# Kernel optimization log

Measured on AMD Instinct MI355X. Metric: run time of the kernel, lower is better.

## Reference

```python
import jax, jax.numpy as jnp
import numpy as np
import math

D_MODEL = 512
N_HEADS = 8
D_FF = 2048
E_LAYERS = 2
ENC_IN = 3
MA_K = 25            # moving_avg kernel size
FACTOR = 1
B, L_CYC, CDL = 16, 20, 128
SEQ = L_CYC * CDL    # 2560
TOP_K = int(FACTOR * math.log(SEQ))  # 7
OUTPUT_NUM = 1


def moving_avg(x, k=MA_K):
    # x: [B,S,D]; replicate-pad ends by (k-1)//2, stride-1 mean pool -> length S
    p = (k - 1) // 2
    xp = jnp.concatenate([jnp.repeat(x[:, :1], p, axis=1), x, jnp.repeat(x[:, -1:], p, axis=1)], axis=1)
    c = jnp.cumsum(xp, axis=1)
    c = jnp.concatenate([jnp.zeros_like(c[:, :1]), c], axis=1)
    return (c[:, k:] - c[:, :-k]) / k


def token_embed(x, W):
    # x: [B,S,C], W: [D_MODEL, C, 3]; Conv1d k=3, circular padding, no bias
    xc = jnp.pad(x.transpose(0, 2, 1), ((0, 0), (0, 0), (1, 1)), mode='wrap')
    y = jax.lax.conv_general_dilated(xc, W, (1,), 'VALID', dimension_numbers=('NCH', 'OIH', 'NCH'))
    return y.transpose(0, 2, 1)  # [B,S,D]


def autocorrelation(q, k, v):
    # q,k,v: [B,S,H,E]; FFT autocorrelation + top-k time-delay aggregation (inference path)
    B_, S, H, E = q.shape
    qf = jnp.fft.rfft(q.transpose(0, 2, 3, 1), axis=-1)      # [B,H,E,F]
    kf = jnp.fft.rfft(k.transpose(0, 2, 3, 1), axis=-1)
    corr = jnp.fft.irfft(qf * jnp.conj(kf), n=S, axis=-1)    # [B,H,E,S]
    vals = v.transpose(0, 2, 3, 1)                           # [B,H,E,S]
    mean_corr = corr.mean(axis=(1, 2))                       # [B,S]
    weights, delay = jax.lax.top_k(mean_corr, TOP_K)         # [B,K]
    w = jax.nn.softmax(weights, axis=-1)

    def agg_one(v_b, d_b, w_b):
        # roll by -delay == gather values at index (t + delay) mod S
        out = jnp.zeros_like(v_b)
        for i in range(TOP_K):
            out = out + jnp.roll(v_b, -d_b[i], axis=-1) * w_b[i]
        return out

    V = jax.vmap(agg_one)(vals, delay, w)                    # [B,H,E,S]
    return V.transpose(0, 3, 1, 2)                           # [B,S,H,E]


def my_layernorm(x, g, b):
    # LayerNorm over last dim, then subtract the per-series (time) mean
    mu = x.mean(-1, keepdims=True)
    var = ((x - mu) ** 2).mean(-1, keepdims=True)
    xh = (x - mu) / jnp.sqrt(var + 1e-5) * g + b
    return xh - xh.mean(axis=1, keepdims=True)


def encoder_layer(x, Wq, bq, Wk, bk, Wv, bv, Wo, bo, Wc1, Wc2):
    B_, S, D = x.shape
    H, E = N_HEADS, D // N_HEADS
    q = (x @ Wq + bq).reshape(B_, S, H, E)
    k = (x @ Wk + bk).reshape(B_, S, H, E)
    v = (x @ Wv + bv).reshape(B_, S, H, E)
    att = autocorrelation(q, k, v).reshape(B_, S, D)
    x = x + (att @ Wo + bo)
    x = x - moving_avg(x)                                    # series_decomp1: residual part
    y = jax.nn.gelu(x @ Wc1, approximate=False) @ Wc2        # 1x1 convs, no bias
    z = x + y
    return z - moving_avg(z)                                 # series_decomp2


def setup_inputs() -> dict:
    key = jax.random.key(0)
    ks = jax.random.split(key, 12)
    s = 0.02
    rn = lambda k, shape: jax.random.normal(k, shape, dtype=jnp.float32) * s
    return {
        'cycle_curve_data': jax.random.normal(ks[0], (B, L_CYC, ENC_IN, CDL), dtype=jnp.float32),
        'curve_attn_mask': jnp.ones((B, L_CYC), dtype=jnp.float32),
        'W_emb': rn(ks[1], (D_MODEL, ENC_IN, 3)),
        'Wq': rn(ks[2], (E_LAYERS, D_MODEL, D_MODEL)),
        'bq': jnp.zeros((E_LAYERS, D_MODEL), jnp.float32),
        'Wk': rn(ks[3], (E_LAYERS, D_MODEL, D_MODEL)),
        'bk': jnp.zeros((E_LAYERS, D_MODEL), jnp.float32),
        'Wv': rn(ks[4], (E_LAYERS, D_MODEL, D_MODEL)),
        'bv': jnp.zeros((E_LAYERS, D_MODEL), jnp.float32),
        'Wo': rn(ks[5], (E_LAYERS, D_MODEL, D_MODEL)),
        'bo': jnp.zeros((E_LAYERS, D_MODEL), jnp.float32),
        'Wc1': rn(ks[6], (E_LAYERS, D_MODEL, D_FF)),
        'Wc2': rn(ks[7], (E_LAYERS, D_FF, D_MODEL)),
        'gamma': jnp.ones((D_MODEL,), jnp.float32),
        'beta': jnp.zeros((D_MODEL,), jnp.float32),
        'Wp': rn(ks[8], (D_MODEL * SEQ, OUTPUT_NUM)),
        'bp': jnp.zeros((OUTPUT_NUM,), jnp.float32),
    }


def reference(cycle_curve_data, curve_attn_mask, W_emb, Wq, bq, Wk, bk, Wv, bv, Wo, bo, Wc1, Wc2, gamma, beta, Wp, bp):
    mask = curve_attn_mask[:, :, None, None]                 # [B,L,1,1]
    x = jnp.where(mask == 0, 0.0, cycle_curve_data)          # zero masked cycles
    Bn = x.shape[0]
    x = x.transpose(0, 1, 3, 2).reshape(Bn, SEQ, ENC_IN)     # [B, L*CDL, NV]
    h = token_embed(x, W_emb)                                # DataEmbedding_wo_pos (x_mark=None, dropout=0)
    for l in range(E_LAYERS):
        h = encoder_layer(h, Wq[l], bq[l], Wk[l], bk[l], Wv[l], bv[l], Wo[l], bo[l], Wc1[l], Wc2[l])
    h = my_layernorm(h, gamma, beta)
    out = jax.nn.gelu(h, approximate=False)
    emb = out.reshape(Bn, -1)
    return emb @ Wp + bp                                     # [B, OUTPUT_NUM]
```

## Files before the change

### kernel.cpp

```cpp
#include <hip/hip_runtime.h>
#include <math.h>

#define BATCH 16
#define L_CYC 20
#define CDL 128
#define SEQ 2560
#define ENC_IN 3
#define DMODEL 512
#define DFF 2048
#define NLAYERS 2
#define TOPK 7
#define MROWS (BATCH*SEQ)
#define SD ((size_t)BATCH * SEQ * DMODEL)
#define FFN_CHUNK 20480
#define CHUNK_D 256
#define DGRP 8
#define FFT_NT 512

typedef short bf16x8 __attribute__((ext_vector_type(8)));
typedef float f32x4 __attribute__((ext_vector_type(4)));

__device__ __forceinline__ float gelu_f(float x) {
    return 0.5f * x * (1.0f + erff(x * 0.70710678118654752f));
}
__device__ __forceinline__ unsigned short f2bf(float f) {
    unsigned int u = __float_as_uint(f);
    u += 0x7fff + ((u >> 16) & 1);
    return (unsigned short)(u >> 16);
}
__device__ __forceinline__ float bf2f(unsigned short h) {
    return __uint_as_float(((unsigned int)h) << 16);
}
__device__ __forceinline__ void xcd_map(int p, int G, int& g, int& n) {
    int a = p >> 3;
    n = a % G;
    g = (a / G) * 8 + (p & 7);
}

__global__ __launch_bounds__(256) void embed_kernel(
    const float* __restrict__ data, const float* __restrict__ mask,
    const float* __restrict__ Wemb, float* __restrict__ h) {
    __shared__ float xv[9];
    size_t idx = (size_t)blockIdx.x * 256 + threadIdx.x;
    size_t r = idx >> 9;
    int s = (int)(r % SEQ);
    int b = (int)(r / SEQ);
    int tid = threadIdx.x;
    if (tid < 9) {
        int t = tid / 3, c = tid % 3;
        int u = s - 1 + t;
        if (u < 0) u += SEQ;
        if (u >= SEQ) u -= SEQ;
        int cyc = u >> 7, pos = u & 127;
        float mk = mask[b * L_CYC + cyc];
        xv[c * 3 + t] = (mk == 0.f) ? 0.f
            : data[(((size_t)b * L_CYC + cyc) * ENC_IN + c) * CDL + pos];
    }
    __syncthreads();
    int dm = idx & (DMODEL - 1);
    float acc = 0.f;
#pragma unroll
    for (int j = 0; j < 9; j++) acc += xv[j] * Wemb[dm * 9 + j];
    h[idx] = acc;
}

__global__ void conv_split_kernel(const float* __restrict__ in,
                                  unsigned short* __restrict__ hi,
                                  unsigned short* __restrict__ lo, size_t n) {
    size_t i = ((size_t)blockIdx.x * 256 + threadIdx.x) * 4;
    if (i >= n) return;
    float4 v = *(const float4*)(in + i);
    float vv[4] = { v.x, v.y, v.z, v.w };
#pragma unroll
    for (int j = 0; j < 4; j++) {
        unsigned short h = f2bf(vv[j]);
        hi[i + j] = h;
        lo[i + j] = f2bf(vv[j] - bf2f(h));
    }
}

__global__ __launch_bounds__(256) void transpose_bf16_kernel(
    const float* __restrict__ W, unsigned short* __restrict__ Wt, int K, int N) {
    __shared__ float t[32][33];
    int n0 = blockIdx.x * 32, k0 = blockIdx.y * 32;
    int c = threadIdx.x & 31, r = threadIdx.x >> 5;
    for (int i = 0; i < 4; i++)
        t[r + i * 8][c] = W[(size_t)(k0 + r + i * 8) * N + n0 + c];
    __syncthreads();
    for (int i = 0; i < 4; i++)
        Wt[(size_t)(n0 + r + i * 8) * K + k0 + c] = f2bf(t[c][r + i * 8]);
}

__global__ __launch_bounds__(256) void transpose_split_stk_kernel(
    const float* __restrict__ W, unsigned short* __restrict__ WtH,
    unsigned short* __restrict__ WtL, int which) {
    __shared__ float t[32][33];
    int n0 = blockIdx.x * 32, k0 = blockIdx.y * 32;
    int c = threadIdx.x & 31, r = threadIdx.x >> 5;
    for (int i = 0; i < 4; i++)
        t[r + i * 8][c] = W[(size_t)(k0 + r + i * 8) * DMODEL + n0 + c];
    __syncthreads();
    for (int i = 0; i < 4; i++) {
        int n = n0 + r + i * 8;
        int row = (n & 255) + ((n >> 8) * 512) + which * 256;
        float v = t[c][r + i * 8];
        unsigned short h = f2bf(v);
        size_t o = (size_t)row * DMODEL + k0 + c;
        WtH[o] = h;
        WtL[o] = f2bf(v - bf2f(h));
    }
}

__global__ void stack_bias_kernel(const float* __restrict__ bq,
                                  const float* __restrict__ bk, float* __restrict__ bstk) {
    int i = blockIdx.x * 256 + threadIdx.x;
    if (i >= 1024) return;
    int c = i >> 9, j = i & 511;
    bstk[i] = (j < 256) ? bq[c * 256 + j] : bk[c * 256 + (j - 256)];
}

__global__ __launch_bounds__(256) void wvo_kernel(
    const float* __restrict__ Wv, const float* __restrict__ Wo,
    float* __restrict__ Wvo) {
    __shared__ float row[DMODEL];
    int k = blockIdx.x;
    int tid = threadIdx.x;
    for (int j = tid; j < DMODEL; j += 256) row[j] = Wv[(size_t)k * DMODEL + j];
    __syncthreads();
    float a0 = 0.f, a1 = 0.f;
    for (int j = 0; j < DMODEL; j++) {
        float wv = row[j];
        a0 += wv * Wo[(size_t)j * DMODEL + tid];
        a1 += wv * Wo[(size_t)j * DMODEL + tid + 256];
    }
    Wvo[(size_t)k * DMODEL + tid] = a0;
    Wvo[(size_t)k * DMODEL + tid + 256] = a1;
}

__global__ void cbias_kernel(const float* __restrict__ bv, const float* __restrict__ Wo,
                             const float* __restrict__ bo, float* __restrict__ cb) {
    int n = blockIdx.x * 256 + threadIdx.x;
    if (n >= DMODEL) return;
    float acc = bo[n];
    for (int j = 0; j < DMODEL; j++) acc += bv[j] * Wo[(size_t)j * DMODEL + n];
    cb[n] = acc;
}

#define BK 32
__global__ __launch_bounds__(256) void gemm_mfma_kernel(
    const unsigned short* __restrict__ A, const unsigned short* __restrict__ Wt,
    const float* __restrict__ bias, const float* res,
    void* Cout, int M, int N, int K, int act, int outMode, int gridN)
{
    __shared__ unsigned short As[128 * 40];
    __shared__ unsigned short Bs[128 * 40];
    int tid = threadIdx.x;
    int wave = tid >> 6, lane = tid & 63;
    int wm = wave & 1, wn = wave >> 1;
    int gblk, nblk;
    xcd_map(blockIdx.x, gridN, gblk, nblk);
    int bm = gblk * 128, bn = nblk * 128;

    int r0 = tid >> 2;
    int koff = (tid & 3) * 8;
    const unsigned short* Ag = A  + (size_t)(bm + r0) * K + koff;
    const unsigned short* Bg = Wt + (size_t)(bn + r0) * K + koff;

    f32x4 acc[4][4] = {};
    int frow = lane & 15, fk = (lane >> 4) * 8;

    for (int k0 = 0; k0 < K; k0 += BK) {
        bf16x8 a0 = *(const bf16x8*)(Ag + k0);
        bf16x8 a1 = *(const bf16x8*)(Ag + (size_t)64 * K + k0);
        bf16x8 b0 = *(const bf16x8*)(Bg + k0);
        bf16x8 b1 = *(const bf16x8*)(Bg + (size_t)64 * K + k0);
        __syncthreads();
        *(bf16x8*)&As[r0 * 40 + koff]        = a0;
        *(bf16x8*)&As[(r0 + 64) * 40 + koff] = a1;
        *(bf16x8*)&Bs[r0 * 40 + koff]        = b0;
        *(bf16x8*)&Bs[(r0 + 64) * 40 + koff] = b1;
        __syncthreads();
        bf16x8 af[4], bfv[4];
#pragma unroll
        for (int mi = 0; mi < 4; mi++)
            af[mi] = *(const bf16x8*)&As[(wm * 64 + mi * 16 + frow) * 40 + fk];
#pragma unroll
        for (int nj = 0; nj < 4; nj++)
            bfv[nj] = *(const bf16x8*)&Bs[(wn * 64 + nj * 16 + frow) * 40 + fk];
#pragma unroll
        for (int mi = 0; mi < 4; mi++)
#pragma unroll
            for (int nj = 0; nj < 4; nj++)
                acc[mi][nj] = __builtin_amdgcn_mfma_f32_16x16x32_bf16(
                    af[mi], bfv[nj], acc[mi][nj], 0, 0, 0);
    }

    int lrow = (lane >> 4) * 4, lcol = lane & 15;
#pragma unroll
    for (int mi = 0; mi < 4; mi++) {
        int row0 = bm + wm * 64 + mi * 16 + lrow;
#pragma unroll
        for (int nj = 0; nj < 4; nj++) {
            int col = bn + wn * 64 + nj * 16 + lcol;
            float bv = bias ? bias[col] : 0.f;
            f32x4 v = acc[mi][nj];
#pragma unroll
            for (int r = 0; r < 4; r++) {
                int row = row0 + r;
                float x = v[r] + bv;
                if (res) x += res[(size_t)row * N + col];
                if (act == 1) x = gelu_f(x);
                if (outMode == 0) ((float*)Cout)[(size_t)row * N + col] = x;
                else              ((unsigned short*)Cout)[(size_t)row * N + col] = f2bf(x);
            }
        }
    }
}

__global__ __launch_bounds__(256) void gemm_qk_split_kernel(
    const unsigned short* __restrict__ Ahi, const unsigned short* __restrict__ Alo,
    const unsigned short* __restrict__ Whi, const unsigned short* __restrict__ Wlo,
    const float* __restrict__ bias, float* __restrict__ Ct, int M, int K, int gridN)
{
    __shared__ unsigned short AsH[128 * 40];
    __shared__ unsigned short AsL[128 * 40];
    __shared__ unsigned short BsH[128 * 40];
    __shared__ unsigned short BsL[128 * 40];
    int tid = threadIdx.x;
    int wave = tid >> 6, lane = tid & 63;
    int wm = wave & 1, wn = wave >> 1;
    int gblk, nblk;
    xcd_map(blockIdx.x, gridN, gblk, nblk);
    int bm = gblk * 128, bn = nblk * 128;

    int r0 = tid >> 2;
    int koff = (tid & 3) * 8;
    const unsigned short* AgH = Ahi + (size_t)(bm + r0) * K + koff;
    const unsigned short* AgL = Alo + (size_t)(bm + r0) * K + koff;
    const unsigned short* BgH = Whi + (size_t)(bn + r0) * K + koff;
    const unsigned short* BgL = Wlo + (size_t)(bn + r0) * K + koff;

    f32x4 acc[4][4] = {};
    int frow = lane & 15, fk = (lane >> 4) * 8;

    for (int k0 = 0; k0 < K; k0 += BK) {
        bf16x8 ah0 = *(const bf16x8*)(AgH + k0);
        bf16x8 ah1 = *(const bf16x8*)(AgH + (size_t)64 * K + k0);
        bf16x8 al0 = *(const bf16x8*)(AgL + k0);
        bf16x8 al1 = *(const bf16x8*)(AgL + (size_t)64 * K + k0);
        bf16x8 bh0 = *(const bf16x8*)(BgH + k0);
        bf16x8 bh1 = *(const bf16x8*)(BgH + (size_t)64 * K + k0);
        bf16x8 bl0 = *(const bf16x8*)(BgL + k0);
        bf16x8 bl1 = *(const bf16x8*)(BgL + (size_t)64 * K + k0);
        __syncthreads();
        *(bf16x8*)&AsH[r0 * 40 + koff]        = ah0;
        *(bf16x8*)&AsH[(r0 + 64) * 40 + koff] = ah1;
        *(bf16x8*)&AsL[r0 * 40 + koff]        = al0;
        *(bf16x8*)&AsL[(r0 + 64) * 40 + koff] = al1;
        *(bf16x8*)&BsH[r0 * 40 + koff]        = bh0;
        *(bf16x8*)&BsH[(r0 + 64) * 40 + koff] = bh1;
        *(bf16x8*)&BsL[r0 * 40 + koff]        = bl0;
        *(bf16x8*)&BsL[(r0 + 64) * 40 + koff] = bl1;
        __syncthreads();
        bf16x8 afh[4], afl[4], bfh[4], bfl[4];
#pragma unroll
        for (int mi = 0; mi < 4; mi++) {
            int o = (wm * 64 + mi * 16 + frow) * 40 + fk;
            afh[mi] = *(const bf16x8*)&AsH[o];
            afl[mi] = *(const bf16x8*)&AsL[o];
        }
#pragma unroll
        for (int nj = 0; nj < 4; nj++) {
            int o = (wn * 64 + nj * 16 + frow) * 40 + fk;
            bfh[nj] = *(const bf16x8*)&BsH[o];
            bfl[nj] = *(const bf16x8*)&BsL[o];
        }
#pragma unroll
        for (int mi = 0; mi < 4; mi++)
#pragma unroll
            for (int nj = 0; nj < 4; nj++) {
                acc[mi][nj] = __builtin_amdgcn_mfma_f32_16x16x32_bf16(
                    afh[mi], bfh[nj], acc[mi][nj], 0, 0, 0);
                acc[mi][nj] = __builtin_amdgcn_mfma_f32_16x16x32_bf16(
                    afh[mi], bfl[nj], acc[mi][nj], 0, 0, 0);
                acc[mi][nj] = __builtin_amdgcn_mfma_f32_16x16x32_bf16(
                    afl[mi], bfh[nj], acc[mi][nj], 0, 0, 0);
            }
    }

    int lrow = (lane >> 4) * 4, lcol = lane & 15;
#pragma unroll
    for (int mi = 0; mi < 4; mi++) {
        int row0 = bm + wm * 64 + mi * 16 + lrow;
#pragma unroll
        for (int nj = 0; nj < 4; nj++) {
            int col = bn + wn * 64 + nj * 16 + lcol;
            float bv = bias ? bias[col] : 0.f;
            f32x4 v = acc[mi][nj];
#pragma unroll
            for (int r = 0; r < 4; r++)
                Ct[(size_t)col * M + row0 + r] = v[r] + bv;
        }
    }
}

template<int NT>
__device__ void fft2560(float2* bufA, float2* bufB, const float2* w512, int tid) {
    const float w5r[5] = { 1.f,  0.30901699437494742f, -0.80901699437494742f,
                          -0.80901699437494742f,  0.30901699437494742f };
    const float w5i[5] = { 0.f, -0.95105651629515357f, -0.58778525229247312f,
                           0.58778525229247312f,  0.95105651629515357f };
    __syncthreads();
    const float TWO_PI = 6.283185307179586f;
    for (int j = tid; j < SEQ; j += NT) {
        int k1 = j >> 9, n2 = j & 511;
        float ar = 0.f, ai = 0.f;
        for (int n1 = 0; n1 < 5; n1++) {
            int m = (n1 * k1) % 5;
            float2 x = bufA[n1 * 512 + n2];
            ar += x.x * w5r[m] - x.y * w5i[m];
            ai += x.x * w5i[m] + x.y * w5r[m];
        }
        float ang = -TWO_PI * (float)(n2 * k1) / 2560.0f;
        float sn, cs;
        sincosf(ang, &sn, &cs);
        bufB[j] = make_float2(ar * cs - ai * sn, ar * sn + ai * cs);
    }
    __syncthreads();
    float2* X = bufB;
    float2* Y = bufA;
    int n = 512, logs = 0;
    for (int st = 0; st < 9; st++) {
        int m = n >> 1;
        int s = 1 << logs;
        for (int t = tid; t < 1280; t += NT) {
            int sub = t >> 8;
            int r = t & 255;
            int p = r >> logs;
            int q = r & (s - 1);
            int base = sub << 9;
            float2 a = X[base + q + s * p];
            float2 b = X[base + q + s * (p + m)];
            float2 sum = make_float2(a.x + b.x, a.y + b.y);
            float2 dif = make_float2(a.x - b.x, a.y - b.y);
            float2 w = w512[p << logs];
            Y[base + q + s * (2 * p)]     = sum;
            Y[base + q + s * (2 * p + 1)] = make_float2(dif.x * w.x - dif.y * w.y,
                                                        dif.x * w.y + dif.y * w.x);
        }
        __syncthreads();
        float2* tmp = X; X = Y; Y = tmp;
        n >>= 1; logs++;
    }
}

__global__ __launch_bounds__(FFT_NT) void fft_fwd_kernel(
    const float* __restrict__ qt, const float* __restrict__ kt, float* __restrict__ Z)
{
    __shared__ float2 bufA[SEQ];
    __shared__ float2 bufB[SEQ];
    __shared__ float2 w512[256];
    int d0 = blockIdx.x * DGRP;
    int b = blockIdx.y;
    int tid = threadIdx.x;
    if (tid < 256) {
        float sn, cs;
        sincosf(-6.283185307179586f * (float)tid / 512.0f, &sn, &cs);
        w512[tid] = make_float2(cs, sn);
    }
    float accR[5], accI[5];
#pragma unroll
    for (int j = 0; j < 5; j++) { accR[j] = 0.f; accI[j] = 0.f; }

    for (int col = 0; col < DGRP; col++) {
        const float* qcol = qt + (size_t)(d0 + col) * MROWS + (size_t)b * SEQ;
        const float* kcol = kt + (size_t)(d0 + col) * MROWS + (size_t)b * SEQ;
        __syncthreads();
        for (int i = tid; i < SEQ; i += FFT_NT)
            bufA[i] = make_float2(qcol[i], kcol[i]);
        fft2560<FFT_NT>(bufA, bufB, w512, tid);
#pragma unroll
        for (int j = 0; j < 5; j++) {
            int f = tid + FFT_NT * j;
            int fpos = (f % 5) * 512 + (f / 5);
            int g = f ? (SEQ - f) : 0;
            int gpos = (g % 5) * 512 + (g / 5);
            float2 Z1 = bufA[fpos], Z2 = bufA[gpos];
            accR[j] += 0.5f * (Z1.x * Z2.y + Z1.y * Z2.x);
            accI[j] += 0.25f * ((Z1.x * Z1.x + Z1.y * Z1.y)
                              - (Z2.x * Z2.x + Z2.y * Z2.y));
        }
    }
#pragma unroll
    for (int j = 0; j < 5; j++) {
        int f = tid + FFT_NT * j;
        int fpos = (f % 5) * 512 + (f / 5);
        atomicAdd(&Z[((size_t)b * SEQ + fpos) * 2 + 0], accR[j]);
        atomicAdd(&Z[((size_t)b * SEQ + fpos) * 2 + 1], accI[j]);
    }
}

__global__ __launch_bounds__(FFT_NT) void fft_inv_kernel(
    const float* __restrict__ Z, float* __restrict__ mc)
{
    __shared__ float2 bufA[SEQ];
    __shared__ float2 bufB[SEQ];
    __shared__ float2 w512[256];
    int b = blockIdx.x;
    int tid = threadIdx.x;
    if (tid < 256) {
        float sn, cs;
        sincosf(-6.283185307179586f * (float)tid / 512.0f, &sn, &cs);
        w512[tid] = make_float2(cs, sn);
    }
    for (int i = tid; i < SEQ; i += FFT_NT) {
        int k1 = i % 5, k2 = i / 5;
        float zr = Z[((size_t)b * SEQ + k1 * 512 + k2) * 2 + 0];
        float zi = Z[((size_t)b * SEQ + k1 * 512 + k2) * 2 + 1];
        bufA[i] = make_float2(zr, -zi);
    }
    fft2560<FFT_NT>(bufA, bufB, w512, tid);
    const float scale = 1.0f / (2560.0f * 512.0f);
    for (int j = tid; j < SEQ; j += FFT_NT) {
        int k1 = j >> 9, k2 = j & 511;
        mc[(size_t)b * SEQ + k1 + 5 * k2] = bufA[j].x * scale;
    }
}

__global__ __launch_bounds__(256) void topk_kernel(
    const float* __restrict__ mc, float* __restrict__ wts, int* __restrict__ dels)
{
    __shared__ float cv[SEQ];
    __shared__ float rv[256];
    __shared__ int   ri[256];
    __shared__ float topv[TOPK];
    __shared__ int   topi[TOPK];
    int b = blockIdx.x, tid = threadIdx.x;
    for (int i = tid; i < SEQ; i += 256) cv[i] = mc[(size_t)b * SEQ + i];
    __syncthreads();
    for (int it = 0; it < TOPK; it++) {
        float bv = -2e30f; int bi = 1 << 30;
        for (int i = tid; i < SEQ; i += 256) {
            float v = cv[i];
            if (v > bv || (v == bv && i < bi)) { bv = v; bi = i; }
        }
        rv[tid] = bv; ri[tid] = bi;
        __syncthreads();
        for (int off = 128; off > 0; off >>= 1) {
            if (tid < off) {
                float v2 = rv[tid + off]; int i2 = ri[tid + off];
                if (v2 > rv[tid] || (v2 == rv[tid] && i2 < ri[tid])) {
                    rv[tid] = v2; ri[tid] = i2;
                }
            }
            __syncthreads();
        }
        if (tid == 0) { topv[it] = rv[0]; topi[it] = ri[0]; cv[ri[0]] = -1e30f; }
        __syncthreads();
    }
    if (tid == 0) {
        float mx = topv[0];
        float e[TOPK], ssum = 0.f;
        for (int i = 0; i < TOPK; i++) { e[i] = expf(topv[i] - mx); ssum += e[i]; }
        for (int i = 0; i < TOPK; i++) {
            wts[b * TOPK + i] = e[i] / ssum;
            dels[b * TOPK + i] = topi[i];
        }
    }
}

__global__ void agg_res_kernel(const float* __restrict__ u, const float* __restrict__ x,
                               const float* __restrict__ cb,
                               const float* __restrict__ wts, const int* __restrict__ dels,
                               float* __restrict__ x1) {
    size_t idx = (size_t)blockIdx.x * 256 + threadIdx.x;
    if (idx >= SD) return;
    int d = idx & (DMODEL - 1);
    size_t r = idx >> 9;
    int s = (int)(r % SEQ);
    int b = (int)(r / SEQ);
    float acc = cb[d] + x[idx];
    for (int i = 0; i < TOPK; i++) {
        int del = dels[b * TOPK + i];
        float w = wts[b * TOPK + i];
        int ss = s + del; if (ss >= SEQ) ss -= SEQ;
        acc += w * u[((size_t)b * SEQ + ss) * DMODEL + d];
    }
    x1[idx] = acc;
}

#define MA_MODE_PLAIN 0
#define MA_MODE_BF    1
#define MA_MODE_SPLIT 2
template<int MODE>
__device__ __forceinline__ void ma_run_body(
    const float* __restrict__ x, float* __restrict__ out,
    unsigned short* __restrict__ o1, unsigned short* __restrict__ o2)
{
    int tid = threadIdx.x;
    int s0 = blockIdx.x * 128;
    int d  = blockIdx.y * 256 + tid;
    int b  = blockIdx.z;
    const float* xb = x + (size_t)b * SEQ * DMODEL + d;
    float sum = 0.f;
#pragma unroll
    for (int j = -12; j <= 12; j++) {
        int ss = s0 + j;
        ss = ss < 0 ? 0 : (ss > SEQ - 1 ? SEQ - 1 : ss);
        sum += xb[(size_t)ss * DMODEL];
    }
    for (int s = s0; s < s0 + 128; s++) {
        float v = xb[(size_t)s * DMODEL] - sum * (1.0f / 25.0f);
        size_t o = ((size_t)b * SEQ + s) * DMODEL + d;
        out[o] = v;
        if (MODE == MA_MODE_BF) {
            o1[o] = f2bf(v);
        } else if (MODE == MA_MODE_SPLIT) {
            unsigned short h = f2bf(v);
            o1[o] = h;
            o2[o] = f2bf(v - bf2f(h));
        }
        int add = s + 13; if (add > SEQ - 1) add = SEQ - 1;
        int sub = s - 12; if (sub < 0) sub = 0;
        sum += xb[(size_t)add * DMODEL] - xb[(size_t)sub * DMODEL];
    }
}
__global__ __launch_bounds__(256) void ma_sub_kernel(
    const float* __restrict__ x, float* __restrict__ out) {
    ma_run_body<MA_MODE_PLAIN>(x, out, nullptr, nullptr);
}
__global__ __launch_bounds__(256) void ma_sub_bf_kernel(
    const float* __restrict__ x, float* __restrict__ out,
    unsigned short* __restrict__ obf) {
    ma_run_body<MA_MODE_BF>(x, out, obf, nullptr);
}
__global__ __launch_bounds__(256) void ma_sub_split_kernel(
    const float* __restrict__ x, float* __restrict__ out,
    unsigned short* __restrict__ hi, unsigned short* __restrict__ lo) {
    ma_run_body<MA_MODE_SPLIT>(x, out, hi, lo);
}

__global__ __launch_bounds__(256) void ln_kernel(
    const float* __restrict__ x, const float* __restrict__ g,
    const float* __restrict__ be, float* __restrict__ xh)
{
    int row = blockIdx.x;
    int tid = threadIdx.x;
    __shared__ float red[256];
    const float* xr = x + (size_t)row * DMODEL;
    float v0 = xr[tid], v1 = xr[tid + 256];
    red[tid] = v0 + v1;
    __syncthreads();
    for (int off = 128; off > 0; off >>= 1) {
        if (tid < off) red[tid] += red[tid + off];
        __syncthreads();
    }
    float mu = red[0] / (float)DMODEL;
    __syncthreads();
    float d0 = v0 - mu, d1 = v1 - mu;
    red[tid] = d0 * d0 + d1 * d1;
    __syncthreads();
    for (int off = 128; off > 0; off >>= 1) {
        if (tid < off) red[tid] += red[tid + off];
        __syncthreads();
    }
    float inv = rsqrtf(red[0] / (float)DMODEL + 1e-5f);
    xh[(size_t)row * DMODEL + tid]       = d0 * inv * g[tid] + be[tid];
    xh[(size_t)row * DMODEL + tid + 256] = d1 * inv * g[tid + 256] + be[tid + 256];
}

__global__ __launch_bounds__(256) void colmean_kernel(
    const float* __restrict__ xh, float* __restrict__ cm) {
    int idx = blockIdx.x * 256 + threadIdx.x;
    int d = idx & (DMODEL - 1), b = idx >> 9;
    int s0 = blockIdx.y * 128;
    float acc = 0.f;
    for (int s = s0; s < s0 + 128; s++)
        acc += xh[((size_t)b * SEQ + s) * DMODEL + d];
    atomicAdd(&cm[idx], acc * (1.0f / (float)SEQ));
}

__global__ __launch_bounds__(256) void final_kernel(
    const float* __restrict__ xh, const float* __restrict__ cm,
    const float* __restrict__ Wp, const float* __restrict__ bp,
    float* __restrict__ out)
{
    int b = blockIdx.y, chunk = blockIdx.x;
    int tid = threadIdx.x;
    const size_t per = (size_t)SEQ * DMODEL / 64;
    size_t start = (size_t)chunk * per;
    float acc = 0.f;
    for (size_t i = start + tid; i < start + per; i += 256) {
        int d = (int)(i & (DMODEL - 1));
        float v = xh[(size_t)b * SEQ * DMODEL + i] - cm[b * DMODEL + d];
        acc += gelu_f(v) * Wp[i];
    }
    __shared__ float red[256];
    red[tid] = acc;
    __syncthreads();
    for (int off = 128; off > 0; off >>= 1) {
        if (tid < off) red[tid] += red[tid + off];
        __syncthreads();
    }
    if (tid == 0) {
        atomicAdd(&out[b], red[0]);
        if (chunk == 0) atomicAdd(&out[b], bp[0]);
    }
}

extern "C" void kernel_launch(void* const* d_in, const int* in_sizes, int n_in,
                              void* d_out, int out_size, void* d_ws, size_t ws_size,
                              hipStream_t stream) {
    const float* data  = (const float*)d_in[0];
    const float* mask  = (const float*)d_in[1];
    const float* Wemb  = (const float*)d_in[2];
    const float* Wq    = (const float*)d_in[3];
    const float* bq    = (const float*)d_in[4];
    const float* Wk    = (const float*)d_in[5];
    const float* bk    = (const float*)d_in[6];
    const float* Wv    = (const float*)d_in[7];
    const float* bv    = (const float*)d_in[8];
    const float* Wo    = (const float*)d_in[9];
    const float* bo    = (const float*)d_in[10];
    const float* Wc1   = (const float*)d_in[11];
    const float* Wc2   = (const float*)d_in[12];
    const float* gamma = (const float*)d_in[13];
    const float* beta  = (const float*)d_in[14];
    const float* Wp    = (const float*)d_in[15];
    const float* bp    = (const float*)d_in[16];
    float* out = (float*)d_out;

    float* buf0 = (float*)d_ws;
    float* buf1 = buf0 + SD;
    float* buf2 = buf1 + SD;

    unsigned short* WstkH = (unsigned short*)(buf2 + SD);
    unsigned short* WstkL = WstkH + 2 * DMODEL * DMODEL;
    unsigned short* Wvot  = WstkL + 2 * DMODEL * DMODEL;
    unsigned short* Wc1t  = Wvot + DMODEL * DMODEL;
    unsigned short* Wc2t  = Wc1t + (size_t)DMODEL * DFF;
    float* WvoF = (float*)(Wc2t + (size_t)DMODEL * DFF);
    float* CB   = WvoF + (size_t)DMODEL * DMODEL;
    float* Bstk = CB + DMODEL;
    float* Zb = Bstk + 1024;
    float* MC = Zb + (size_t)BATCH * SEQ * 2;
    float* WT = MC + (size_t)BATCH * SEQ;
    int*   DL = (int*)(WT + BATCH * TOPK);
    float* CM = (float*)(DL + BATCH * TOPK);

    const int NB  = (int)((SD + 255) / 256);
    const int NB4 = (int)((SD / 4 + 255) / 256);
    dim3 gMA(SEQ / 128, 2, BATCH);

    float* X  = buf0;
    float* HL = buf1;
    float* S  = buf2;

    embed_kernel<<<NB, 256, 0, stream>>>(data, mask, Wemb, X);
    conv_split_kernel<<<NB4, 256, 0, stream>>>(
        X, (unsigned short*)HL + SD, (unsigned short*)HL, SD);

    const int gSqBlocks = (MROWS / 128) * (DMODEL / 128);
    const int gF1Blocks = (FFN_CHUNK / 128) * (DFF / 128);
    const int gF2Blocks = (FFN_CHUNK / 128) * (DMODEL / 128);

    for (int l = 0; l < NLAYERS; l++) {
        const float* wq = Wq + (size_t)l * DMODEL * DMODEL;
        const float* wk = Wk + (size_t)l * DMODEL * DMODEL;
        const float* wv = Wv + (size_t)l * DMODEL * DMODEL;
        const float* wo = Wo + (size_t)l * DMODEL * DMODEL;
        const float* bqL = bq + (size_t)l * DMODEL;
        const float* bkL = bk + (size_t)l * DMODEL;
        const float* bvL = bv + (size_t)l * DMODEL;
        const float* boL = bo + (size_t)l * DMODEL;
        const float* wc1 = Wc1 + (size_t)l * DMODEL * DFF;
        const float* wc2 = Wc2 + (size_t)l * DFF * DMODEL;

        unsigned short* Lbf = (unsigned short*)HL;
        unsigned short* Hbf = Lbf + SD;
        float* qtf = S;
        float* ktf = S + (size_t)MROWS * CHUNK_D;

        dim3 gT(DMODEL / 32, DMODEL / 32);
        transpose_split_stk_kernel<<<gT, 256, 0, stream>>>(wq, WstkH, WstkL, 0);
        transpose_split_stk_kernel<<<gT, 256, 0, stream>>>(wk, WstkH, WstkL, 1);
        stack_bias_kernel<<<4, 256, 0, stream>>>(bqL, bkL, Bstk);
        wvo_kernel<<<DMODEL, 256, 0, stream>>>(wv, wo, WvoF);
        transpose_bf16_kernel<<<gT, 256, 0, stream>>>(WvoF, Wvot, DMODEL, DMODEL);
        cbias_kernel<<<2, 256, 0, stream>>>(bvL, wo, boL, CB);
        transpose_bf16_kernel<<<dim3(DFF / 32, DMODEL / 32), 256, 0, stream>>>(wc1, Wc1t, DMODEL, DFF);
        transpose_bf16_kernel<<<dim3(DMODEL / 32, DFF / 32), 256, 0, stream>>>(wc2, Wc2t, DFF, DMODEL);

        hipMemsetAsync(Zb, 0, (size_t)BATCH * SEQ * 2 * sizeof(float), stream);
        for (int c = 0; c < DMODEL / CHUNK_D; c++) {
            gemm_qk_split_kernel<<<gSqBlocks, 256, 0, stream>>>(
                Hbf, Lbf, WstkH + (size_t)c * 512 * DMODEL,
                WstkL + (size_t)c * 512 * DMODEL, Bstk + c * 512,
                S, MROWS, DMODEL, DMODEL / 128);
            fft_fwd_kernel<<<dim3(CHUNK_D / DGRP, BATCH), FFT_NT, 0, stream>>>(qtf, ktf, Zb);
        }
        fft_inv_kernel<<<BATCH, FFT_NT, 0, stream>>>(Zb, MC);
        topk_kernel<<<BATCH, 256, 0, stream>>>(MC, WT, DL);

        gemm_mfma_kernel<<<gSqBlocks, 256, 0, stream>>>(Hbf, Wvot, nullptr, nullptr, S,
                                                        MROWS, DMODEL, DMODEL, 0, 0,
                                                        DMODEL / 128);
        agg_res_kernel<<<NB, 256, 0, stream>>>(S, X, CB, WT, DL, HL);
        ma_sub_bf_kernel<<<gMA, 256, 0, stream>>>(HL, X, (unsigned short*)S);
        for (int c = 0; c < MROWS / FFN_CHUNK; c++) {
            const unsigned short* x2c = (unsigned short*)S + (size_t)c * FFN_CHUNK * DMODEL;
            float* xz = X + (size_t)c * FFN_CHUNK * DMODEL;
            gemm_mfma_kernel<<<gF1Blocks, 256, 0, stream>>>(x2c, Wc1t, nullptr, nullptr,
                                                            (unsigned short*)HL,
                                                            FFN_CHUNK, DFF, DMODEL, 1, 1,
                                                            DFF / 128);
            gemm_mfma_kernel<<<gF2Blocks, 256, 0, stream>>>((unsigned short*)HL, Wc2t,
                                                            nullptr, xz, xz,
                                                            FFN_CHUNK, DMODEL, DFF, 0, 0,
                                                            DMODEL / 128);
        }
        if (l + 1 < NLAYERS)
            ma_sub_split_kernel<<<gMA, 256, 0, stream>>>(
                X, S, (unsigned short*)HL + SD, (unsigned short*)HL);
        else
            ma_sub_kernel<<<gMA, 256, 0, stream>>>(X, S);
        float* tmp = X; X = S; S = tmp;
    }

    ln_kernel<<<MROWS, 256, 0, stream>>>(X, gamma, beta, HL);
    hipMemsetAsync(CM, 0, (size_t)BATCH * DMODEL * sizeof(float), stream);
    colmean_kernel<<<dim3(32, 20), 256, 0, stream>>>(HL, CM);
    hipMemsetAsync(out, 0, (size_t)out_size * sizeof(float), stream);
    final_kernel<<<dim3(64, BATCH), 256, 0, stream>>>(HL, CM, Wp, bp, out);
}
```

Measured before the change: 2.272 ms.

## Rewrite FFT-2560 core with radix-4 stages, swizzled LDS and precomputed twiddles

Replaces the nine radix-2 stages of the 512-point sub-FFTs with four radix-4 stages plus one final radix-2 stage. This halves the number of barrier-separated LDS passes. LDS indices go through an XOR swizzle to cut bank conflicts. The per-element sincosf in the radix-5 pass is replaced by per-thread twiddles computed once, and the radix-5 pass is unrolled so each thread handles its five inputs in registers. The cost is more index arithmetic and a new output ordering that must line up with the later consumers.

```diff
diff --git a/kernel.cpp b/kernel.cpp
--- a/kernel.cpp
+++ b/kernel.cpp
@@ -304,54 +304,90 @@
     }
 }
 
+__device__ __forceinline__ int swz(int a) { return a ^ ((a >> 4) & 15); }
+
+template<int LOGS, int NT>
+__device__ __forceinline__ void radix4_stage(const float2* __restrict__ X,
+                                             float2* __restrict__ Y,
+                                             const float2* __restrict__ w512x,
+                                             int tid) {
+    const int s = 1 << LOGS;
+    for (int t = tid; t < 640; t += NT) {
+        int sub = t >> 7, r = t & 127;
+        int base = sub << 9;
+        int q = r & (s - 1);
+        int ps = r - q;
+        float2 x0 = X[swz(base + r)];
+        float2 x1 = X[swz(base + r + 128)];
+        float2 x2 = X[swz(base + r + 256)];
+        float2 x3 = X[swz(base + r + 384)];
+        float A0r = x0.x + x2.x, A0i = x0.y + x2.y;
+        float B0r = x1.x + x3.x, B0i = x1.y + x3.y;
+        float A1r = x0.x - x2.x, A1i = x0.y - x2.y;
+        float B1r = x1.x - x3.x, B1i = x1.y - x3.y;
+        float2 w1 = w512x[ps];
+        float w2r = w1.x * w1.x - w1.y * w1.y;
+        float w2i = 2.0f * w1.x * w1.y;
+        float w3r = w2r * w1.x - w2i * w1.y;
+        float w3i = w2r * w1.y + w2i * w1.x;
+        float u1r = A1r + B1i, u1i = A1i - B1r;
+        float u2r = A0r - B0r, u2i = A0i - B0i;
+        float u3r = A1r - B1i, u3i = A1i + B1r;
+        int ob = base + q + 4 * ps;
+        Y[swz(ob)]         = make_float2(A0r + B0r, A0i + B0i);
+        Y[swz(ob + s)]     = make_float2(u1r * w1.x - u1i * w1.y,
+                                         u1r * w1.y + u1i * w1.x);
+        Y[swz(ob + 2 * s)] = make_float2(u2r * w2r - u2i * w2i,
+                                         u2r * w2i + u2i * w2r);
+        Y[swz(ob + 3 * s)] = make_float2(u3r * w3r - u3i * w3i,
+                                         u3r * w3i + u3i * w3r);
+    }
+}
+
 template<int NT>
-__device__ void fft2560(float2* bufA, float2* bufB, const float2* w512, int tid) {
-    const float w5r[5] = { 1.f,  0.30901699437494742f, -0.80901699437494742f,
-                          -0.80901699437494742f,  0.30901699437494742f };
-    const float w5i[5] = { 0.f, -0.95105651629515357f, -0.58778525229247312f,
-                           0.58778525229247312f,  0.95105651629515357f };
-    __syncthreads();
-    const float TWO_PI = 6.283185307179586f;
-    for (int j = tid; j < SEQ; j += NT) {
-        int k1 = j >> 9, n2 = j & 511;
-        float ar = 0.f, ai = 0.f;
-        for (int n1 = 0; n1 < 5; n1++) {
-            int m = (n1 * k1) % 5;
-            float2 x = bufA[n1 * 512 + n2];
-            ar += x.x * w5r[m] - x.y * w5i[m];
-            ai += x.x * w5i[m] + x.y * w5r[m];
-        }
-        float ang = -TWO_PI * (float)(n2 * k1) / 2560.0f;
-        float sn, cs;
-        sincosf(ang, &sn, &cs);
-        bufB[j] = make_float2(ar * cs - ai * sn, ar * sn + ai * cs);
-    }
-    __syncthreads();
-    float2* X = bufB;
-    float2* Y = bufA;
-    int n = 512, logs = 0;
-    for (int st = 0; st < 9; st++) {
-        int m = n >> 1;
-        int s = 1 << logs;
-        for (int t = tid; t < 1280; t += NT) {
-            int sub = t >> 8;
-            int r = t & 255;
-            int p = r >> logs;
-            int q = r & (s - 1);
-            int base = sub << 9;
-            float2 a = X[base + q + s * p];
-            float2 b = X[base + q + s * (p + m)];
-            float2 sum = make_float2(a.x + b.x, a.y + b.y);
-            float2 dif = make_float2(a.x - b.x, a.y - b.y);
-            float2 w = w512[p << logs];
-            Y[base + q + s * (2 * p)]     = sum;
-            Y[base + q + s * (2 * p + 1)] = make_float2(dif.x * w.x - dif.y * w.y,
-                                                        dif.x * w.y + dif.y * w.x);
-        }
-        __syncthreads();
-        float2* tmp = X; X = Y; Y = tmp;
-        n >>= 1; logs++;
-    }
+__device__ void fft2560(float2* bufA, float2* bufB, const float2* w512x,
+                        const float2* tw, int tid) {
+    __syncthreads();
+    {
+        const float w5r[5] = { 1.f,  0.30901699437494742f, -0.80901699437494742f,
+                              -0.80901699437494742f,  0.30901699437494742f };
+        const float w5i[5] = { 0.f, -0.95105651629515357f, -0.58778525229247312f,
+                               0.58778525229247312f,  0.95105651629515357f };
+        float2 x[5];
+#pragma unroll
+        for (int n1 = 0; n1 < 5; n1++) x[n1] = bufA[swz(n1 * 512 + tid)];
+#pragma unroll
+        for (int k1 = 0; k1 < 5; k1++) {
+            float ar = 0.f, ai = 0.f;
+#pragma unroll
+            for (int n1 = 0; n1 < 5; n1++) {
+                int m = (n1 * k1) % 5;
+                ar += x[n1].x * w5r[m] - x[n1].y * w5i[m];
+                ai += x[n1].x * w5i[m] + x[n1].y * w5r[m];
+            }
+            if (k1 == 0) {
+                bufB[swz(tid)] = make_float2(ar, ai);
+            } else {
+                float2 w = tw[k1 - 1];
+                bufB[swz(k1 * 512 + tid)] =
+                    make_float2(ar * w.x - ai * w.y, ar * w.y + ai * w.x);
+            }
+        }
+    }
+    __syncthreads();
+    radix4_stage<0, NT>(bufB, bufA, w512x, tid); __syncthreads();
+    radix4_stage<2, NT>(bufA, bufB, w512x, tid); __syncthreads();
+    radix4_stage<4, NT>(bufB, bufA, w512x, tid); __syncthreads();
+    radix4_stage<6, NT>(bufA, bufB, w512x, tid); __syncthreads();
+    for (int t = tid; t < 1280; t += NT) {
+        int sub = t >> 8, q = t & 255;
+        int base = sub << 9;
+        float2 a = bufB[swz(base + q)];
+        float2 b = bufB[swz(base + q + 256)];
+        bufA[swz(base + q)]       = make_float2(a.x + b.x, a.y + b.y);
+        bufA[swz(base + q + 256)] = make_float2(a.x - b.x, a.y - b.y);
+    }
+    __syncthreads();
 }
 
 __global__ __launch_bounds__(FFT_NT) void fft_fwd_kernel(
@@ -359,14 +395,21 @@
 {
     __shared__ float2 bufA[SEQ];
     __shared__ float2 bufB[SEQ];
-    __shared__ float2 w512[256];
+    __shared__ float2 w512x[512];
     int d0 = blockIdx.x * DGRP;
     int b = blockIdx.y;
     int tid = threadIdx.x;
-    if (tid < 256) {
+    {
         float sn, cs;
         sincosf(-6.283185307179586f * (float)tid / 512.0f, &sn, &cs);
-        w512[tid] = make_float2(cs, sn);
+        w512x[tid] = make_float2(cs, sn);
+    }
+    float2 tw[4];
+#pragma unroll
+    for (int k1 = 1; k1 <= 4; k1++) {
+        float sn, cs;
+        sincosf(-2.4543692606170259e-3f * (float)(k1 * tid), &sn, &cs);
+        tw[k1 - 1] = make_float2(cs, sn);
     }
     float accR[5], accI[5];
 #pragma unroll
@@ -377,15 +420,15 @@
         const float* kcol = kt + (size_t)(d0 + col) * MROWS + (size_t)b * SEQ;
         __syncthreads();
         for (int i = tid; i < SEQ; i += FFT_NT)
-            bufA[i] = make_float2(qcol[i], kcol[i]);
-        fft2560<FFT_NT>(bufA, bufB, w512, tid);
+            bufA[swz(i)] = make_float2(qcol[i], kcol[i]);
+        fft2560<FFT_NT>(bufA, bufB, w512x, tw, tid);
 #pragma unroll
         for (int j = 0; j < 5; j++) {
             int f = tid + FFT_NT * j;
             int fpos = (f % 5) * 512 + (f / 5);
             int g = f ? (SEQ - f) : 0;
             int gpos = (g % 5) * 512 + (g / 5);
-            float2 Z1 = bufA[fpos], Z2 = bufA[gpos];
+            float2 Z1 = bufA[swz(fpos)], Z2 = bufA[swz(gpos)];
             accR[j] += 0.5f * (Z1.x * Z2.y + Z1.y * Z2.x);
             accI[j] += 0.25f * ((Z1.x * Z1.x + Z1.y * Z1.y)
                               - (Z2.x * Z2.x + Z2.y * Z2.y));
@@ -405,25 +448,32 @@
 {
     __shared__ float2 bufA[SEQ];
     __shared__ float2 bufB[SEQ];
-    __shared__ float2 w512[256];
+    __shared__ float2 w512x[512];
     int b = blockIdx.x;
     int tid = threadIdx.x;
-    if (tid < 256) {
+    {
         float sn, cs;
         sincosf(-6.283185307179586f * (float)tid / 512.0f, &sn, &cs);
-        w512[tid] = make_float2(cs, sn);
+        w512x[tid] = make_float2(cs, sn);
+    }
+    float2 tw[4];
+#pragma unroll
+    for (int k1 = 1; k1 <= 4; k1++) {
+        float sn, cs;
+        sincosf(-2.4543692606170259e-3f * (float)(k1 * tid), &sn, &cs);
+        tw[k1 - 1] = make_float2(cs, sn);
     }
     for (int i = tid; i < SEQ; i += FFT_NT) {
         int k1 = i % 5, k2 = i / 5;
         float zr = Z[((size_t)b * SEQ + k1 * 512 + k2) * 2 + 0];
         float zi = Z[((size_t)b * SEQ + k1 * 512 + k2) * 2 + 1];
-        bufA[i] = make_float2(zr, -zi);
-    }
-    fft2560<FFT_NT>(bufA, bufB, w512, tid);
+        bufA[swz(i)] = make_float2(zr, -zi);
+    }
+    fft2560<FFT_NT>(bufA, bufB, w512x, tw, tid);
     const float scale = 1.0f / (2560.0f * 512.0f);
     for (int j = tid; j < SEQ; j += FFT_NT) {
         int k1 = j >> 9, k2 = j & 511;
-        mc[(size_t)b * SEQ + k1 + 5 * k2] = bufA[j].x * scale;
+        mc[(size_t)b * SEQ + k1 + 5 * k2] = bufA[swz(j)].x * scale;
     }
 }
 
```

Result: faster. 2.170 ms (-4.5%).
